# Kernel tuning notes

Hardware: AMD Instinct MI355X
Metric: run time of the kernel (lower is better)

Reference implementation:

```python
import jax, jax.numpy as jnp
import numpy as np


def setup_inputs() -> dict:
    key = jax.random.key(0)
    k1, k2 = jax.random.split(key)
    B, T, D = 16, 512, 384
    x = jax.random.normal(k1, (B, T, D), dtype=jnp.float32)
    durations = jax.random.randint(k2, (B, T), 0, 8, dtype=jnp.int64)
    return {"x": x, "durations": durations, "max_len": 4096}


def reference(x, durations, max_len):
    # x: [B, T, D], durations: [B, T] int, max_len: static int
    # Each phoneme t is repeated durations[b, t] times along the frame axis,
    # then sequences are zero-padded to a common length.
    cum = jnp.cumsum(durations, axis=1)              # [B, T] exclusive upper bounds
    frames = jnp.arange(max_len)                     # [F]
    # frame f belongs to phoneme idx where cum[idx-1] <= f < cum[idx]
    idx = jax.vmap(lambda c: jnp.searchsorted(c, frames, side="right"))(cum)  # [B, F]
    valid = frames[None, :] < cum[:, -1][:, None]    # [B, F] frames past total -> pad
    idx = jnp.minimum(idx, durations.shape[1] - 1)   # clamp out-of-range gather
    out = jnp.take_along_axis(x, idx[:, :, None], axis=1)  # [B, F, D]
    return jnp.where(valid[:, :, None], out, jnp.zeros((), dtype=x.dtype))
```

## Files before the change

kernel.cpp:

```cpp
#include <hip/hip_runtime.h>

#define BB   16
#define TT   512
#define FF   4096
#define DD4  96
#define FPT  16
#define TILES (FF / FPT)
#define NTHR 256
#define NXCD 8

typedef float f4 __attribute__((ext_vector_type(4)));

__global__ __launch_bounds__(TT) void build_idx_kernel(
    const int* __restrict__ dur, int* __restrict__ fidx) {
    const int b = blockIdx.x;
    const int t = threadIdx.x;
    int* fb = fidx + b * FF;

#pragma unroll
    for (int k = 0; k < FF / TT; ++k) fb[k * TT + t] = -1;

    const int d = dur[b * TT + t];

    int v = d;
#pragma unroll
    for (int off = 1; off < 64; off <<= 1) {
        int u = __shfl_up(v, off, 64);
        if ((t & 63) >= off) v += u;
    }

    __shared__ int wsum[TT / 64];
    const int wid = t >> 6;
    if ((t & 63) == 63) wsum[wid] = v;
    __syncthreads();

    int base = 0;
#pragma unroll
    for (int w = 0; w < TT / 64 - 1; ++w)
        if (w < wid) base += wsum[w];

    const int cum = v + base;
    const int start = cum - d;
    const int end = cum < FF ? cum : FF;
    for (int f = start; f < end; ++f) fb[f] = t;
}

__global__ __launch_bounds__(NTHR) void gather_kernel(
    const f4* __restrict__ x, const int* __restrict__ fidx,
    f4* __restrict__ out) {
    int bid = blockIdx.x;
    bid = (bid & (NXCD - 1)) * (BB * TILES / NXCD) + (bid >> 3);

    const int b    = bid / TILES;
    const int tile = bid - b * TILES;
    const int t    = threadIdx.x;
    const int fl   = t >> 4;
    const int c0   = t & 15;
    const int f    = tile * FPT + fl;

    const int idx = fidx[b * FF + f];
    f4* dst = out + ((size_t)b * FF + f) * DD4;

    if (idx >= 0) {
        const f4* src = x + ((size_t)b * TT + idx) * DD4;
#pragma unroll
        for (int k = 0; k < 6; ++k) {
            f4 v = src[c0 + 16 * k];
            __builtin_nontemporal_store(v, &dst[c0 + 16 * k]);
        }
    } else {
        const f4 z = {0.f, 0.f, 0.f, 0.f};
#pragma unroll
        for (int k = 0; k < 6; ++k)
            __builtin_nontemporal_store(z, &dst[c0 + 16 * k]);
    }
}

extern "C" void kernel_launch(void* const* d_in, const int* in_sizes, int n_in,
                              void* d_out, int out_size, void* d_ws, size_t ws_size,
                              hipStream_t stream) {
    const float* x = (const float*)d_in[0];
    const int* dur = (const int*)d_in[1];
    int* fidx = (int*)d_ws;

    build_idx_kernel<<<BB, TT, 0, stream>>>(dur, fidx);
    gather_kernel<<<BB * TILES, NTHR, 0, stream>>>(
        (const f4*)x, fidx, (f4*)d_out);
}
```

Before: 124.1 us.

## Fuse index build into gather kernel with per-block scan and binary search

Replaces the two-kernel pipeline (a scatter-based frame index build followed by a gather) with one kernel. Each block recomputes the prefix sum of durations for its batch in shared memory, then binary-searches it to find the phoneme for each of its 64 frames. This removes a kernel launch, the workspace index array traffic and the serial per-thread scatter loop. In exchange every block redoes the 512-element scan and pays about nine shared-memory search steps per frame.

```diff
diff --git a/kernel.cpp b/kernel.cpp
--- a/kernel.cpp
+++ b/kernel.cpp
@@ -1,78 +1,88 @@
 #include <hip/hip_runtime.h>
 
-#define BB   16
-#define TT   512
-#define FF   4096
-#define DD4  96
-#define FPT  16
-#define TILES (FF / FPT)
-#define NTHR 256
-#define NXCD 8
+#define BB    16
+#define TT    512
+#define FF    4096
+#define DD4   96
+#define NTHR  256
+#define FPB   64
+#define CHUNKS (FF / FPB)
+#define NBLK  (BB * CHUNKS)
+#define NXCD  8
 
 typedef float f4 __attribute__((ext_vector_type(4)));
 
-__global__ __launch_bounds__(TT) void build_idx_kernel(
-    const int* __restrict__ dur, int* __restrict__ fidx) {
-    const int b = blockIdx.x;
-    const int t = threadIdx.x;
-    int* fb = fidx + b * FF;
+__global__ __launch_bounds__(NTHR) void lenreg_kernel(
+    const f4* __restrict__ x, const int* __restrict__ dur,
+    f4* __restrict__ out) {
 
-#pragma unroll
-    for (int k = 0; k < FF / TT; ++k) fb[k * TT + t] = -1;
+    int bid = blockIdx.x;
+    bid = (bid & (NXCD - 1)) * (NBLK / NXCD) + (bid >> 3);
 
-    const int d = dur[b * TT + t];
+    const int b     = bid >> 6;
+    const int chunk = bid & (CHUNKS - 1);
+    const int t     = threadIdx.x;
+    const int lane  = t & 63;
+    const int wid   = t >> 6;
 
-    int v = d;
+    __shared__ int s_cum[TT];
+    __shared__ int s_ws[NTHR / 64];
+
+    const int2 dd = ((const int2*)(dur + b * TT))[t];
+    int v = dd.x + dd.y;
 #pragma unroll
     for (int off = 1; off < 64; off <<= 1) {
         int u = __shfl_up(v, off, 64);
-        if ((t & 63) >= off) v += u;
+        if (lane >= off) v += u;
+    }
+    if (lane == 63) s_ws[wid] = v;
+    __syncthreads();
+    int base = 0;
+#pragma unroll
+    for (int w = 0; w < NTHR / 64 - 1; ++w)
+        if (w < wid) base += s_ws[w];
+    const int c1 = base + v;
+    s_cum[2 * t]     = c1 - dd.y;
+    s_cum[2 * t + 1] = c1;
+    __syncthreads();
+
+    const int total = s_cum[TT - 1];
+    const int fl    = t >> 4;
+    const int c0    = t & 15;
+    const int fbase = chunk * FPB;
+
+    int idx0, idx1, idx2, idx3;
+    {
+        int ii[4];
+#pragma unroll
+        for (int it = 0; it < 4; ++it) {
+            const int f = fbase + it * 16 + fl;
+            int idx = 0;
+#pragma unroll
+            for (int step = 256; step > 0; step >>= 1) {
+                if (idx + step <= TT && s_cum[idx + step - 1] <= f) idx += step;
+            }
+            ii[it] = idx;
+        }
+        idx0 = ii[0]; idx1 = ii[1]; idx2 = ii[2]; idx3 = ii[3];
     }
 
-    __shared__ int wsum[TT / 64];
-    const int wid = t >> 6;
-    if ((t & 63) == 63) wsum[wid] = v;
-    __syncthreads();
-
-    int base = 0;
 #pragma unroll
-    for (int w = 0; w < TT / 64 - 1; ++w)
-        if (w < wid) base += wsum[w];
-
-    const int cum = v + base;
-    const int start = cum - d;
-    const int end = cum < FF ? cum : FF;
-    for (int f = start; f < end; ++f) fb[f] = t;
-}
-
-__global__ __launch_bounds__(NTHR) void gather_kernel(
-    const f4* __restrict__ x, const int* __restrict__ fidx,
-    f4* __restrict__ out) {
-    int bid = blockIdx.x;
-    bid = (bid & (NXCD - 1)) * (BB * TILES / NXCD) + (bid >> 3);
-
-    const int b    = bid / TILES;
-    const int tile = bid - b * TILES;
-    const int t    = threadIdx.x;
-    const int fl   = t >> 4;
-    const int c0   = t & 15;
-    const int f    = tile * FPT + fl;
-
-    const int idx = fidx[b * FF + f];
-    f4* dst = out + ((size_t)b * FF + f) * DD4;
-
-    if (idx >= 0) {
-        const f4* src = x + ((size_t)b * TT + idx) * DD4;
+    for (int it = 0; it < 4; ++it) {
+        const int idx = (it == 0) ? idx0 : (it == 1) ? idx1 : (it == 2) ? idx2 : idx3;
+        const int f   = fbase + it * 16 + fl;
+        f4* dst = out + ((size_t)b * FF + f) * DD4;
+        if (f < total) {
+            const f4* src = x + ((size_t)b * TT + idx) * DD4;
 #pragma unroll
-        for (int k = 0; k < 6; ++k) {
-            f4 v = src[c0 + 16 * k];
-            __builtin_nontemporal_store(v, &dst[c0 + 16 * k]);
+            for (int k = 0; k < 6; ++k)
+                __builtin_nontemporal_store(src[c0 + 16 * k], &dst[c0 + 16 * k]);
+        } else {
+            const f4 z = {0.f, 0.f, 0.f, 0.f};
+#pragma unroll
+            for (int k = 0; k < 6; ++k)
+                __builtin_nontemporal_store(z, &dst[c0 + 16 * k]);
         }
-    } else {
-        const f4 z = {0.f, 0.f, 0.f, 0.f};
-#pragma unroll
-        for (int k = 0; k < 6; ++k)
-            __builtin_nontemporal_store(z, &dst[c0 + 16 * k]);
     }
 }
 
@@ -81,9 +91,8 @@
                               hipStream_t stream) {
     const float* x = (const float*)d_in[0];
     const int* dur = (const int*)d_in[1];
-    int* fidx = (int*)d_ws;
+    (void)d_ws; (void)ws_size;
 
-    build_idx_kernel<<<BB, TT, 0, stream>>>(dur, fidx);
-    gather_kernel<<<BB * TILES, NTHR, 0, stream>>>(
-        (const f4*)x, fidx, (f4*)d_out);
+    lenreg_kernel<<<NBLK, NTHR, 0, stream>>>(
+        (const f4*)x, dur, (f4*)d_out);
 }
```

New measurement: 126.3 us. About the same (+1.8%).
